# Optimization experiments

Hardware: AMD Instinct MI355X
Metric: run time of the kernel (lower is better)

Reference implementation:

```python
import jax, jax.numpy as jnp
import numpy as np

B, N, K, CIN, COUT = 2, 8192, 16, 64, 64


def setup_inputs() -> dict:
    key = jax.random.key(0)
    ks = jax.random.split(key, 12)
    w = lambda k, shape: jax.random.normal(k, shape, jnp.float32) * 0.02
    return dict(
        pos=jax.random.normal(ks[0], (B, N, 3), jnp.float32),
        features=jax.random.normal(ks[1], (B, N, CIN), jnp.float32),
        emb_w=w(ks[2], (CIN, COUT)), emb_b=jnp.zeros((COUT,), jnp.float32),
        wq=w(ks[3], (COUT, COUT)), wk=w(ks[4], (COUT, COUT)), wv=w(ks[5], (COUT, COUT)),
        pe_w1=w(ks[6], (3, COUT)), pe_b1=jnp.zeros((COUT,), jnp.float32),
        pe_w2=w(ks[7], (COUT, COUT)), pe_b2=jnp.zeros((COUT,), jnp.float32),
        at_w1=w(ks[8], (COUT, COUT)), at_b1=jnp.zeros((COUT,), jnp.float32),
        at_w2=w(ks[9], (COUT, COUT)), at_b2=jnp.zeros((COUT,), jnp.float32),
        out_w=w(ks[10], (COUT, CIN)), out_b=jnp.zeros((CIN,), jnp.float32),
    )


def _gather(x, idx):
    # x: [B, N, C], idx: [B, N, K] -> [B, N, K, C]
    return jax.vmap(lambda xb, ib: xb[ib])(x, idx)


def reference(pos, features, emb_w, emb_b, wq, wk, wv,
              pe_w1, pe_b1, pe_w2, pe_b2,
              at_w1, at_b1, at_w2, at_b2, out_w, out_b):
    # KNN: squared pairwise distances, take k smallest (includes self)
    sq = jnp.sum(pos * pos, axis=-1)                                  # [B, N]
    d2 = sq[:, :, None] + sq[:, None, :] - 2.0 * jnp.einsum('bnd,bmd->bnm', pos, pos)
    _, knn_idx = jax.lax.top_k(-d2, K)                                # [B, N, K]

    # recenter_groups: neighbor positions relative to query point
    grouped_pos = _gather(pos, knn_idx) - pos[:, :, None, :]          # [B, N, K, 3]

    x = features @ emb_w + emb_b                                      # [B, N, COUT]
    q = x @ wq                                                        # [B, N, COUT]
    k = _gather(x @ wk, knn_idx)                                      # [B, N, K, COUT]
    v = _gather(x @ wv, knn_idx)                                      # [B, N, K, COUT]

    # mlp_posenc: Linear(3,C) -> ReLU -> Linear(C,C)
    posenc = jax.nn.relu(grouped_pos @ pe_w1 + pe_b1) @ pe_w2 + pe_b2  # [B, N, K, COUT]

    # mlp_attn on (q - k + posenc), softmax over neighbor axis (dim=-2)
    h = q[:, :, None, :] - k + posenc
    attn = jax.nn.relu(h @ at_w1 + at_b1) @ at_w2 + at_b2
    attn = jax.nn.softmax(attn / np.float32(np.sqrt(COUT)), axis=-2)

    result = jnp.einsum('bmnf,bmnf->bmf', attn, v + posenc)           # [B, N, COUT]
    return result @ out_w + out_b + features                          # [B, N, CIN]
```

## Files before the change

### kernel.cpp

```cpp
#include <hip/hip_runtime.h>
#include <hip/hip_bf16.h>

#define BB 2
#define NN 8192
#define SPL 16
#define CAND (NN/SPL)
#define NPTS (BB*NN)

#define POS4_OFF 0u
#define PART_OFF 65536u
#define IDX_OFF  4259840u
#define WT_OFF   4521984u
#define QB_OFF   4530176u
#define KVB_OFF  5578752u

typedef __attribute__((ext_vector_type(8))) short bf16x8;
typedef __attribute__((ext_vector_type(4))) float f32x4;

__device__ __forceinline__ unsigned umn(unsigned a, unsigned b) {
#if __has_builtin(__builtin_elementwise_min)
  return __builtin_elementwise_min(a, b);
#else
  return a < b ? a : b;
#endif
}
__device__ __forceinline__ unsigned umx(unsigned a, unsigned b) {
#if __has_builtin(__builtin_elementwise_max)
  return __builtin_elementwise_max(a, b);
#else
  return a < b ? b : a;
#endif
}

__device__ inline unsigned short f2bf(float x) {
  __hip_bfloat16 b = __float2bfloat16(x);
  return *(unsigned short*)&b;
}

#define HCOL(c, j) ((((((c) >> 3) + (j)) & 7) << 3) | ((c) & 7))

__global__ __launch_bounds__(256) void mega1(
    const float* __restrict__ pos, const float* __restrict__ feat,
    const float* __restrict__ emb_w, const float* __restrict__ emb_b,
    const float* __restrict__ wq, const float* __restrict__ wk,
    const float* __restrict__ wv,
    const float* __restrict__ pe_w2, const float* __restrict__ at_w1,
    const float* __restrict__ at_w2, const float* __restrict__ out_w,
    float* __restrict__ ws)
{
  __shared__ __align__(16) float smem[6144];
  const int tid = threadIdx.x;
  const int bx = blockIdx.x;
  float* pos4 = ws + POS4_OFF;
  unsigned* part = (unsigned*)ws + PART_OFF;
  float* qg = ws + QB_OFF;
  unsigned* kvp = (unsigned*)ws + KVB_OFF;

  if (bx < 1024) {
    constexpr int OE[63][2] = {
      {0,1},{2,3},{4,5},{6,7},{8,9},{10,11},{12,13},{14,15},
      {0,2},{1,3},{4,6},{5,7},{8,10},{9,11},{12,14},{13,15},
      {1,2},{5,6},{9,10},{13,14},
      {0,4},{1,5},{2,6},{3,7},{8,12},{9,13},{10,14},{11,15},
      {2,4},{3,5},{10,12},{11,13},
      {1,2},{3,4},{5,6},{9,10},{11,12},{13,14},
      {0,8},{1,9},{2,10},{3,11},{4,12},{5,13},{6,14},{7,15},
      {4,8},{5,9},{6,10},{7,11},
      {2,4},{3,5},{6,8},{7,9},{10,12},{11,13},
      {1,2},{3,4},{5,6},{7,8},{9,10},{11,12},{13,14}
    };
    const int g = (bx & 63) * 256 + tid;
    const int s = bx >> 6;
    const int bu = __builtin_amdgcn_readfirstlane(g >> 13);
    const float qx = pos[g * 3 + 0], qy = pos[g * 3 + 1], qz = pos[g * 3 + 2];
    const float* __restrict__ cp = pos + (bu * NN + s * CAND) * 3;
    const unsigned jb = (unsigned)(s * CAND);
    unsigned m[16];
#pragma unroll
    for (int i = 0; i < 16; i++) m[i] = 0xFFFFFFFFu;
    for (int j0 = 0; j0 < CAND; j0 += 16) {
      float c[48];
#pragma unroll
      for (int i = 0; i < 48; i++) c[i] = cp[j0 * 3 + i];
      unsigned b[16];
#pragma unroll
      for (int i = 0; i < 16; i++) {
        float dx = c[i * 3 + 0] - qx;
        float dy = c[i * 3 + 1] - qy;
        float dz = c[i * 3 + 2] - qz;
        float d2 = fmaf(dx, dx, fmaf(dy, dy, dz * dz));
        b[i] = (__float_as_uint(d2) & 0xFFFFE000u) | (jb + (unsigned)(j0 + i));
      }
#pragma unroll
      for (int cc = 0; cc < 63; cc++) {
        const int x = OE[cc][0], y = OE[cc][1];
        unsigned lo = umn(b[x], b[y]);
        unsigned hi = umx(b[x], b[y]);
        b[x] = hi; b[y] = lo;
      }
#pragma unroll
      for (int i = 0; i < 16; i++) m[i] = umn(m[i], b[i]);
#pragma unroll
      for (int d = 8; d; d >>= 1) {
#pragma unroll
        for (int i = 0; i < 16; i++) {
          if ((i & d) == 0) {
            const int l = i | d;
            unsigned lo = umn(m[i], m[l]);
            unsigned hi = umx(m[i], m[l]);
            m[i] = lo; m[l] = hi;
          }
        }
      }
    }
#pragma unroll
    for (int i = 0; i < 16; i++)
      part[(unsigned)(s * 16 + i) * NPTS + (unsigned)g] = m[i];
  } else if (bx < 1536) {
    float* wl = smem;
    float* xl = smem + 4096;
    const int vb = bx - 1024;
    const int col = tid & 63;
    const int rg = tid >> 6;
    const int row0 = vb * 32 + rg * 8;
    const int rowu = __builtin_amdgcn_readfirstlane(row0);
    if (tid < 32) {
      const int p = vb * 32 + tid;
      float x = pos[p * 3 + 0], y = pos[p * 3 + 1], z = pos[p * 3 + 2];
      float4 v = {x, y, z, 0.f};
      ((float4*)pos4)[p] = v;
    }
    for (int i = tid; i < 4096; i += 256) wl[i] = emb_w[i];
    __syncthreads();
    {
      float acc[8];
      float bias = emb_b[col];
#pragma unroll
      for (int r = 0; r < 8; r++) acc[r] = bias;
      for (int c = 0; c < 64; c++) {
        float w = wl[c * 64 + col];
        const float* fp = feat + rowu * 64 + c;
#pragma unroll
        for (int r = 0; r < 8; r++) acc[r] = fmaf(fp[r * 64], w, acc[r]);
      }
#pragma unroll
      for (int r = 0; r < 8; r++) xl[(rg * 8 + r) * 64 + col] = acc[r];
    }
    __syncthreads();
    for (int i = tid; i < 4096; i += 256) wl[i] = wq[i];
    __syncthreads();
    {
      float aq[8];
#pragma unroll
      for (int r = 0; r < 8; r++) aq[r] = 0.f;
      for (int c = 0; c < 64; c++) {
        float w = wl[c * 64 + col];
#pragma unroll
        for (int r = 0; r < 8; r++)
          aq[r] = fmaf(xl[(rg * 8 + r) * 64 + c], w, aq[r]);
      }
#pragma unroll
      for (int r = 0; r < 8; r++) qg[(row0 + r) * 64 + col] = aq[r];
    }
    __syncthreads();
    for (int i = tid; i < 4096; i += 256) wl[i] = wk[i];
    __syncthreads();
    float ak[8];
    {
#pragma unroll
      for (int r = 0; r < 8; r++) ak[r] = 0.f;
      for (int c = 0; c < 64; c++) {
        float w = wl[c * 64 + col];
#pragma unroll
        for (int r = 0; r < 8; r++)
          ak[r] = fmaf(xl[(rg * 8 + r) * 64 + c], w, ak[r]);
      }
    }
    __syncthreads();
    for (int i = tid; i < 4096; i += 256) wl[i] = wv[i];
    __syncthreads();
    {
      float av[8];
#pragma unroll
      for (int r = 0; r < 8; r++) av[r] = 0.f;
      for (int c = 0; c < 64; c++) {
        float w = wl[c * 64 + col];
#pragma unroll
        for (int r = 0; r < 8; r++)
          av[r] = fmaf(xl[(rg * 8 + r) * 64 + c], w, av[r]);
      }
#pragma unroll
      for (int r = 0; r < 8; r++)
        kvp[(row0 + r) * 64 + col] =
            ((unsigned)f2bf(av[r]) << 16) | (unsigned)f2bf(ak[r]);
    }
  } else {
    const int t = (bx - 1536) * 256 + tid;
    const float* s;
    switch (t >> 12) {
      case 0: s = pe_w2; break;
      case 1: s = at_w1; break;
      case 2: s = at_w2; break;
      default: s = out_w; break;
    }
    const int idx = t & 4095, f = idx >> 6, c = idx & 63;
    ((unsigned short*)(ws + WT_OFF))[t] = f2bf(s[c * 64 + f]);
  }
}

__global__ __launch_bounds__(256) void s3_merge(const float* __restrict__ ws_ro,
                                                int* __restrict__ knn_idx)
{
  const unsigned* part = (const unsigned*)ws_ro + PART_OFF;
  const int g = blockIdx.x * 256 + threadIdx.x;
  unsigned run[16];
#pragma unroll
  for (int i = 0; i < 16; i++) run[i] = part[i * NPTS + g];
#pragma unroll
  for (int l = 1; l < SPL; l++) {
#pragma unroll
    for (int i = 0; i < 16; i++)
      run[i] = umn(run[i], part[(l * 16 + 15 - i) * NPTS + g]);
#pragma unroll
    for (int d = 8; d; d >>= 1) {
#pragma unroll
      for (int i = 0; i < 16; i++) {
        if ((i & d) == 0) {
          const int l2 = i | d;
          unsigned lo = umn(run[i], run[l2]);
          unsigned hi = umx(run[i], run[l2]);
          run[i] = lo; run[l2] = hi;
        }
      }
    }
  }
  const int base = (g >> 13) * NN;
  int outv[16];
#pragma unroll
  for (int i = 0; i < 16; i++) outv[i] = base + (int)(run[i] & 0x1FFFu);
  int4* o = (int4*)(knn_idx + g * 16);
  o[0] = make_int4(outv[0], outv[1], outv[2], outv[3]);
  o[1] = make_int4(outv[4], outv[5], outv[6], outv[7]);
  o[2] = make_int4(outv[8], outv[9], outv[10], outv[11]);
  o[3] = make_int4(outv[12], outv[13], outv[14], outv[15]);
}

__device__ inline void mv(const unsigned short* hm, const bf16x8 B[4][2],
                          const float bias[4], int ln, int s0, int s1,
                          f32x4 acc[4])
{
  bf16x8 a0 = *(const bf16x8*)(hm + ln * 64 + s0);
  bf16x8 a1 = *(const bf16x8*)(hm + ln * 64 + s1);
#pragma unroll
  for (int t = 0; t < 4; t++) {
    f32x4 a = {bias[t], bias[t], bias[t], bias[t]};
    a = __builtin_amdgcn_mfma_f32_16x16x32_bf16(a0, B[t][0], a, 0, 0, 0);
    a = __builtin_amdgcn_mfma_f32_16x16x32_bf16(a1, B[t][1], a, 0, 0, 0);
    acc[t] = a;
  }
}

__global__ __launch_bounds__(256, 2) void s4_attn(
    const float* __restrict__ ws_ro, const float* __restrict__ feat,
    const float* __restrict__ pe_w1, const float* __restrict__ pe_b1,
    const float* __restrict__ pe_b2, const float* __restrict__ at_b1,
    const float* __restrict__ at_b2, const float* __restrict__ out_b,
    const int* __restrict__ knn, float* __restrict__ out)
{
  __shared__ unsigned short hma[4][1024];
  __shared__ unsigned short resm[1024];
  const float* pos4 = ws_ro + POS4_OFF;
  const float* qg = ws_ro + QB_OFF;
  const unsigned* kvp = (const unsigned*)ws_ro + KVB_OFF;
  const unsigned short* wt = (const unsigned short*)(ws_ro + WT_OFF);

  const int tid = threadIdx.x;
  const int wid = tid >> 6, lane = tid & 63;
  const int ln = lane & 15, quad = lane >> 4;
  unsigned short* hm = hma[wid];
  const int s0 = ((quad + ln) & 7) << 3;
  const int s1 = ((4 + quad + ln) & 7) << 3;

  bf16x8 Bf[3][4][2];
#pragma unroll
  for (int m = 0; m < 3; m++)
#pragma unroll
    for (int t = 0; t < 4; t++)
#pragma unroll
      for (int ks = 0; ks < 2; ks++)
        Bf[m][t][ks] = *(const bf16x8*)(wt + m * 4096 + (t * 16 + ln) * 64 +
                                        ks * 32 + quad * 8);
  bf16x8 bo[2];
#pragma unroll
  for (int ks = 0; ks < 2; ks++)
    bo[ks] = *(const bf16x8*)(wt + 3 * 4096 + (wid * 16 + ln) * 64 +
                              ks * 32 + quad * 8);

  float pw10 = pe_w1[lane], pw11 = pe_w1[64 + lane], pw12 = pe_w1[128 + lane];
  float pb1 = pe_b1[lane];
  float bpe[4], ba1[4], ba2[4];
#pragma unroll
  for (int t = 0; t < 4; t++) {
    bpe[t] = pe_b2[t * 16 + ln];
    ba1[t] = at_b1[t * 16 + ln];
    ba2[t] = at_b2[t * 16 + ln];
  }
  const float4* pp4 = (const float4*)pos4;

  const int p0 = blockIdx.x * 16 + wid * 4;
  const int ps0 = __builtin_amdgcn_readfirstlane(p0);
  int4 cur[4];
  {
    const int4* ip4 = (const int4*)(knn + ps0 * 16);
#pragma unroll
    for (int u = 0; u < 4; u++) cur[u] = ip4[u];
  }

  for (int pp = 0; pp < 4; pp++) {
    const int p = p0 + pp;
    const int ps = __builtin_amdgcn_readfirstlane(p);
    int jj[16];
#pragma unroll
    for (int u = 0; u < 4; u++) {
      jj[u*4+0] = cur[u].x; jj[u*4+1] = cur[u].y;
      jj[u*4+2] = cur[u].z; jj[u*4+3] = cur[u].w;
    }
    int4 nxt[4];
    {
      const int pn = (pp < 3) ? (ps + 1) : ps;
      const int4* np4 = (const int4*)(knn + pn * 16);
#pragma unroll
      for (int u = 0; u < 4; u++) nxt[u] = np4[u];
    }
    unsigned kvw[4][4];
#pragma unroll
    for (int r = 0; r < 4; r++) {
      const unsigned* kp = kvp + jj[quad * 4 + r] * 64 + ln;
#pragma unroll
      for (int t = 0; t < 4; t++) kvw[r][t] = kp[t * 16];
    }
    float qv[4];
#pragma unroll
    for (int t = 0; t < 4; t++) qv[t] = qg[p * 64 + t * 16 + ln];

    const float4 mp = pp4[ps];
#pragma unroll
    for (int j = 0; j < 16; j++) {
      const float4 np = pp4[jj[j]];
      float h1 = fmaf(np.z - mp.z, pw12,
                 fmaf(np.y - mp.y, pw11,
                 fmaf(np.x - mp.x, pw10, pb1)));
      hm[j * 64 + HCOL(lane, j)] = f2bf(fmaxf(h1, 0.f));
    }
    f32x4 accp[4];
    mv(hm, Bf[0], bpe, ln, s0, s1, accp);
    float vpe[4][4];
#pragma unroll
    for (int r = 0; r < 4; r++) {
      const int j = quad * 4 + r;
#pragma unroll
      for (int t = 0; t < 4; t++) {
        const unsigned w = kvw[r][t];
        float kf = __uint_as_float(w << 16);
        float vf = __uint_as_float(w & 0xFFFF0000u);
        float pe = accp[t][r];
        vpe[t][r] = vf + pe;
        hm[j * 64 + HCOL(t * 16 + ln, j)] = f2bf(qv[t] - kf + pe);
      }
    }
    f32x4 acch[4];
    mv(hm, Bf[1], ba1, ln, s0, s1, acch);
#pragma unroll
    for (int t = 0; t < 4; t++)
#pragma unroll
      for (int r = 0; r < 4; r++) {
        const int j = quad * 4 + r;
        hm[j * 64 + HCOL(t * 16 + ln, j)] = f2bf(fmaxf(acch[t][r], 0.f));
      }
    f32x4 lg[4];
    mv(hm, Bf[2], ba2, ln, s0, s1, lg);
    const int pb = wid * 4 + pp;
#pragma unroll
    for (int t = 0; t < 4; t++) {
      float e0 = __expf(lg[t][0] * 0.125f);
      float e1 = __expf(lg[t][1] * 0.125f);
      float e2 = __expf(lg[t][2] * 0.125f);
      float e3 = __expf(lg[t][3] * 0.125f);
      float ss = (e0 + e1) + (e2 + e3);
      float dt = fmaf(e3, vpe[t][3], fmaf(e2, vpe[t][2],
                 fmaf(e1, vpe[t][1], e0 * vpe[t][0])));
      ss += __shfl_xor(ss, 16); ss += __shfl_xor(ss, 32);
      dt += __shfl_xor(dt, 16); dt += __shfl_xor(dt, 32);
      float res = dt / ss;
      if (quad == 0) resm[pb * 64 + HCOL(t * 16 + ln, pb)] = f2bf(res);
    }
#pragma unroll
    for (int u = 0; u < 4; u++) cur[u] = nxt[u];
  }
  __syncthreads();
  {
    const int nt = wid;
    float ob = out_b[nt * 16 + ln];
    f32x4 acc = {ob, ob, ob, ob};
#pragma unroll
    for (int ks = 0; ks < 2; ks++) {
      bf16x8 a = *(const bf16x8*)(resm + ln * 64 +
                                  (((ks * 4 + quad + ln) & 7) << 3));
      acc = __builtin_amdgcn_mfma_f32_16x16x32_bf16(a, bo[ks], acc, 0, 0, 0);
    }
#pragma unroll
    for (int r = 0; r < 4; r++) {
      const int pt = blockIdx.x * 16 + quad * 4 + r;
      const int f = nt * 16 + ln;
      out[pt * 64 + f] = acc[r] + feat[pt * 64 + f];
    }
  }
}

extern "C" void kernel_launch(void* const* d_in, const int* in_sizes, int n_in,
                              void* d_out, int out_size, void* d_ws, size_t ws_size,
                              hipStream_t stream)
{
  (void)in_sizes; (void)n_in; (void)out_size; (void)ws_size;
  const float* pos   = (const float*)d_in[0];
  const float* feat  = (const float*)d_in[1];
  const float* emb_w = (const float*)d_in[2];
  const float* emb_b = (const float*)d_in[3];
  const float* wq    = (const float*)d_in[4];
  const float* wk    = (const float*)d_in[5];
  const float* wv    = (const float*)d_in[6];
  const float* pe_w1 = (const float*)d_in[7];
  const float* pe_b1 = (const float*)d_in[8];
  const float* pe_w2 = (const float*)d_in[9];
  const float* pe_b2 = (const float*)d_in[10];
  const float* at_w1 = (const float*)d_in[11];
  const float* at_b1 = (const float*)d_in[12];
  const float* at_w2 = (const float*)d_in[13];
  const float* at_b2 = (const float*)d_in[14];
  const float* out_w = (const float*)d_in[15];
  const float* out_b = (const float*)d_in[16];
  float* ws = (float*)d_ws;

  mega1<<<1600, 256, 0, stream>>>(pos, feat, emb_w, emb_b, wq, wk, wv,
                                  pe_w2, at_w1, at_w2, out_w, ws);
  s3_merge<<<64, 256, 0, stream>>>(ws, (int*)ws + IDX_OFF);
  s4_attn<<<NPTS / 16, 256, 0, stream>>>(ws, feat, pe_w1, pe_b1, pe_b2,
      at_b1, at_b2, out_b, (int*)ws + IDX_OFF, (float*)d_out);
}
```

Measured before the change: 225.1 us.

## Interleave KNN and projection blocks, halve shared memory, prefetch candidates

Reorders block-to-work mapping so each group of 25 blocks mixes 16 KNN-partial blocks, 8 projection blocks and 1 weight-transpose block, so that heterogeneous work is spread across CUs rather than run in phases. Shared memory drops from 24KB to 16KB by staging weight matrices in two halves, which adds extra barriers. The KNN loop now loads the next candidate chunk before the sort network runs, to overlap global loads with compare-swap work at the cost of more live registers.

```diff
diff --git a/kernel.cpp b/kernel.cpp
--- a/kernel.cpp
+++ b/kernel.cpp
@@ -48,15 +48,17 @@
     const float* __restrict__ at_w2, const float* __restrict__ out_w,
     float* __restrict__ ws)
 {
-  __shared__ __align__(16) float smem[6144];
+  __shared__ __align__(16) float smem[4096];
   const int tid = threadIdx.x;
   const int bx = blockIdx.x;
+  const int grp = bx / 25;
+  const int rr = bx - grp * 25;
   float* pos4 = ws + POS4_OFF;
   unsigned* part = (unsigned*)ws + PART_OFF;
   float* qg = ws + QB_OFF;
   unsigned* kvp = (unsigned*)ws + KVB_OFF;
 
-  if (bx < 1024) {
+  if (rr < 16) {
     constexpr int OE[63][2] = {
       {0,1},{2,3},{4,5},{6,7},{8,9},{10,11},{12,13},{14,15},
       {0,2},{1,3},{4,6},{5,7},{8,10},{9,11},{12,14},{13,15},
@@ -69,8 +71,9 @@
       {2,4},{3,5},{6,8},{7,9},{10,12},{11,13},
       {1,2},{3,4},{5,6},{7,8},{9,10},{11,12},{13,14}
     };
-    const int g = (bx & 63) * 256 + tid;
-    const int s = bx >> 6;
+    const int aIdx = grp * 16 + rr;
+    const int g = (aIdx & 63) * 256 + tid;
+    const int s = aIdx >> 6;
     const int bu = __builtin_amdgcn_readfirstlane(g >> 13);
     const float qx = pos[g * 3 + 0], qy = pos[g * 3 + 1], qz = pos[g * 3 + 2];
     const float* __restrict__ cp = pos + (bu * NN + s * CAND) * 3;
@@ -78,10 +81,10 @@
     unsigned m[16];
 #pragma unroll
     for (int i = 0; i < 16; i++) m[i] = 0xFFFFFFFFu;
+    float c[48];
+#pragma unroll
+    for (int i = 0; i < 48; i++) c[i] = cp[i];
     for (int j0 = 0; j0 < CAND; j0 += 16) {
-      float c[48];
-#pragma unroll
-      for (int i = 0; i < 48; i++) c[i] = cp[j0 * 3 + i];
       unsigned b[16];
 #pragma unroll
       for (int i = 0; i < 16; i++) {
@@ -91,6 +94,9 @@
         float d2 = fmaf(dx, dx, fmaf(dy, dy, dz * dz));
         b[i] = (__float_as_uint(d2) & 0xFFFFE000u) | (jb + (unsigned)(j0 + i));
       }
+      const int jn = (j0 + 16 < CAND) ? (j0 + 16) : j0;
+#pragma unroll
+      for (int i = 0; i < 48; i++) c[i] = cp[jn * 3 + i];
 #pragma unroll
       for (int cc = 0; cc < 63; cc++) {
         const int x = OE[cc][0], y = OE[cc][1];
@@ -116,10 +122,10 @@
 #pragma unroll
     for (int i = 0; i < 16; i++)
       part[(unsigned)(s * 16 + i) * NPTS + (unsigned)g] = m[i];
-  } else if (bx < 1536) {
+  } else if (rr < 24) {
     float* wl = smem;
-    float* xl = smem + 4096;
-    const int vb = bx - 1024;
+    float* xl = smem + 2048;
+    const int vb = grp * 8 + (rr - 16);
     const int col = tid & 63;
     const int rg = tid >> 6;
     const int row0 = vb * 32 + rg * 8;
@@ -130,64 +136,73 @@
       float4 v = {x, y, z, 0.f};
       ((float4*)pos4)[p] = v;
     }
-    for (int i = tid; i < 4096; i += 256) wl[i] = emb_w[i];
-    __syncthreads();
     {
       float acc[8];
       float bias = emb_b[col];
 #pragma unroll
       for (int r = 0; r < 8; r++) acc[r] = bias;
-      for (int c = 0; c < 64; c++) {
-        float w = wl[c * 64 + col];
-        const float* fp = feat + rowu * 64 + c;
-#pragma unroll
-        for (int r = 0; r < 8; r++) acc[r] = fmaf(fp[r * 64], w, acc[r]);
+      for (int h = 0; h < 2; h++) {
+        __syncthreads();
+        for (int i = tid; i < 2048; i += 256) wl[i] = emb_w[h * 2048 + i];
+        __syncthreads();
+        for (int cc = 0; cc < 32; cc++) {
+          float w = wl[cc * 64 + col];
+          const float* fp = feat + rowu * 64 + h * 32 + cc;
+#pragma unroll
+          for (int r = 0; r < 8; r++) acc[r] = fmaf(fp[r * 64], w, acc[r]);
+        }
       }
 #pragma unroll
       for (int r = 0; r < 8; r++) xl[(rg * 8 + r) * 64 + col] = acc[r];
     }
-    __syncthreads();
-    for (int i = tid; i < 4096; i += 256) wl[i] = wq[i];
-    __syncthreads();
     {
       float aq[8];
 #pragma unroll
       for (int r = 0; r < 8; r++) aq[r] = 0.f;
-      for (int c = 0; c < 64; c++) {
-        float w = wl[c * 64 + col];
-#pragma unroll
-        for (int r = 0; r < 8; r++)
-          aq[r] = fmaf(xl[(rg * 8 + r) * 64 + c], w, aq[r]);
+      for (int h = 0; h < 2; h++) {
+        __syncthreads();
+        for (int i = tid; i < 2048; i += 256) wl[i] = wq[h * 2048 + i];
+        __syncthreads();
+        for (int cc = 0; cc < 32; cc++) {
+          float w = wl[cc * 64 + col];
+#pragma unroll
+          for (int r = 0; r < 8; r++)
+            aq[r] = fmaf(xl[(rg * 8 + r) * 64 + h * 32 + cc], w, aq[r]);
+        }
       }
 #pragma unroll
       for (int r = 0; r < 8; r++) qg[(row0 + r) * 64 + col] = aq[r];
     }
-    __syncthreads();
-    for (int i = tid; i < 4096; i += 256) wl[i] = wk[i];
-    __syncthreads();
     float ak[8];
     {
 #pragma unroll
       for (int r = 0; r < 8; r++) ak[r] = 0.f;
-      for (int c = 0; c < 64; c++) {
-        float w = wl[c * 64 + col];
-#pragma unroll
-        for (int r = 0; r < 8; r++)
-          ak[r] = fmaf(xl[(rg * 8 + r) * 64 + c], w, ak[r]);
-      }
-    }
-    __syncthreads();
-    for (int i = tid; i < 4096; i += 256) wl[i] = wv[i];
-    __syncthreads();
+      for (int h = 0; h < 2; h++) {
+        __syncthreads();
+        for (int i = tid; i < 2048; i += 256) wl[i] = wk[h * 2048 + i];
+        __syncthreads();
+        for (int cc = 0; cc < 32; cc++) {
+          float w = wl[cc * 64 + col];
+#pragma unroll
+          for (int r = 0; r < 8; r++)
+            ak[r] = fmaf(xl[(rg * 8 + r) * 64 + h * 32 + cc], w, ak[r]);
+        }
+      }
+    }
     {
       float av[8];
 #pragma unroll
       for (int r = 0; r < 8; r++) av[r] = 0.f;
-      for (int c = 0; c < 64; c++) {
-        float w = wl[c * 64 + col];
-#pragma unroll
-        for (int r = 0; r < 8; r++)
-          av[r] = fmaf(xl[(rg * 8 + r) * 64 + c], w, av[r]);
+      for (int h = 0; h < 2; h++) {
+        __syncthreads();
+        for (int i = tid; i < 2048; i += 256) wl[i] = wv[h * 2048 + i];
+        __syncthreads();
+        for (int cc = 0; cc < 32; cc++) {
+          float w = wl[cc * 64 + col];
+#pragma unroll
+          for (int r = 0; r < 8; r++)
+            av[r] = fmaf(xl[(rg * 8 + r) * 64 + h * 32 + cc], w, av[r]);
+        }
       }
 #pragma unroll
       for (int r = 0; r < 8; r++)
@@ -195,7 +210,7 @@
             ((unsigned)f2bf(av[r]) << 16) | (unsigned)f2bf(ak[r]);
     }
   } else {
-    const int t = (bx - 1536) * 256 + tid;
+    const int t = grp * 256 + tid;
     const float* s;
     switch (t >> 12) {
       case 0: s = pe_w2; break;
```

After: 240.0 us. 6.6% more time.
